# Kernel optimization log

Hardware: AMD Instinct MI355X
Metric: run time of the kernel (lower is better)

Reference implementation:

```python
import jax, jax.numpy as jnp
import numpy as np

RESHAPE = 640
NC = 80
TOPK = 10
EPS = 1e-7      # module eps (BCEloss / log clamps)
IOU_EPS = 1e-9  # iou() eps
DIS = 2.5
BS = 16
NUM_GT = 32


def make_anchors():
    pts, strides = [], []
    for s in (8, 16, 32):
        n = RESHAPE // s
        ys, xs = jnp.meshgrid(jnp.arange(n, dtype=jnp.float32),
                              jnp.arange(n, dtype=jnp.float32), indexing='ij')
        pts.append(jnp.stack([xs.ravel(), ys.ravel()], -1))
        strides.append(jnp.full((n * n, 1), float(s), dtype=jnp.float32))
    return jnp.concatenate(pts, 0), jnp.concatenate(strides, 0)


def setup_inputs() -> dict:
    key = jax.random.key(0)
    ks = jax.random.split(key, 8)
    anchor_points, stride_tensor = make_anchors()
    hw = anchor_points.shape[0]

    def rand_boxes(k, lead):
        k1, k2 = jax.random.split(k)
        c = jax.random.uniform(k1, lead + (2,), minval=80.0, maxval=560.0)
        wh = jax.random.uniform(k2, lead + (2,), minval=20.0, maxval=160.0)
        return jnp.concatenate([c - wh / 2, c + wh / 2], -1)

    pred_boxes = rand_boxes(ks[0], (BS, hw))
    gt_boxes = rand_boxes(ks[1], (BS, NUM_GT))
    counts = jax.random.randint(ks[2], (BS,), 8, NUM_GT + 1)
    mask_gt = jnp.arange(NUM_GT)[None, :] < counts[:, None]
    pred_scores = jax.random.uniform(ks[3], (BS, hw, NC)) * 0.98 + 0.01
    pred_conf = jax.random.uniform(ks[4], (BS, hw, 1)) * 0.98 + 0.01
    gt_labels = jax.random.randint(ks[5], (BS, NUM_GT, 1), 0, NC)
    return dict(pred_boxes=pred_boxes, gt_boxes=gt_boxes, mask_gt=mask_gt,
                pred_scores=pred_scores, pred_conf=pred_conf, gt_labels=gt_labels,
                anchor_points=anchor_points, stride_tensor=stride_tensor)


def box_iou(p, g, ciou=False, eps=IOU_EPS):
    # p, g broadcastable [..., 4] in xyxy; matches the torch iou() exactly
    b1x1, b1y1, b1x2, b1y2 = p[..., 0], p[..., 1], p[..., 2], p[..., 3]
    b2x1, b2y1, b2x2, b2y2 = g[..., 0], g[..., 1], g[..., 2], g[..., 3]
    w1, h1 = b1x2 - b1x1, b1y2 - b1y1 + eps
    w2, h2 = b2x2 - b2x1, b2y2 - b2y1 + eps
    inter = (jnp.maximum(jnp.minimum(b1x2, b2x2) - jnp.maximum(b1x1, b2x1), 0.0)
             * jnp.maximum(jnp.minimum(b1y2, b2y2) - jnp.maximum(b1y1, b2y1), 0.0))
    union = w1 * h1 + w2 * h2 - inter + eps
    iou = inter / union
    if ciou:
        cw = jnp.maximum(b1x2, b2x2) - jnp.minimum(b1x1, b2x1)
        ch = jnp.maximum(b1y2, b2y2) - jnp.minimum(b1y1, b2y1)
        c2 = cw ** 2 + ch ** 2 + eps
        d2 = ((b2x1 + b2x2 - b1x1 - b1x2) ** 2 + (b2y1 + b2y2 - b1y1 - b1y2) ** 2) / 4
        v = (4.0 / np.pi ** 2) * (jnp.arctan(w2 / h2) - jnp.arctan(w1 / h1)) ** 2
        alpha = jax.lax.stop_gradient(v / (v - iou + (1.0 + eps)))
        return iou - (d2 / c2 + v * alpha)
    return iou


def _forward(pred_boxes, gt_boxes, mask_gt, pred_scores, pred_conf, gt_labels,
             anchor_points, stride_tensor):
    bs, hw, nc = pred_scores.shape
    G = mask_gt.shape[1]
    dt = pred_boxes.dtype

    apd = (anchor_points + 0.5) * stride_tensor          # (hw, 2)
    gb = gt_boxes[:, :, None, :]                          # (bs, G, 1, 4)
    # strict in-box test
    lt = apd[None, None] - gb[..., :2]
    rb = gb[..., 2:] - apd[None, None]
    in_boxes = (lt > 0).all(-1) & (rb > 0).all(-1)        # (bs, G, hw)
    # center prior (radius 2.5 * stride)
    ctr = (gb[..., :2] + gb[..., 2:]) / 2
    dis = DIS * stride_tensor                             # (hw, 1) -> broadcast (hw, 2)
    lt2 = apd[None, None] - (ctr - dis)
    rb2 = (ctr + dis) - apd[None, None]
    in_centers = (lt2 > 0).all(-1) & (rb2 > 0).all(-1)
    fg = in_boxes | in_centers
    in_both = in_boxes & in_centers

    iou_val = box_iou(pred_boxes[:, None], gt_boxes[:, :, None])   # (bs, G, hw)
    iou_cost = -jnp.log(iou_val + EPS)

    # torch F.binary_cross_entropy with one-hot target zeroed outside fg:
    # sum_c BCE = S + fg * (nll0[label] - nll1[label]), logs clamped at -100
    nll1 = -jnp.maximum(jnp.log(1.0 - pred_scores), -100.0)        # (bs, hw, nc)
    S = nll1.sum(-1)                                               # (bs, hw)
    bidx = jnp.arange(bs)[:, None, None]
    aidx = jnp.arange(hw)[None, None, :]
    lab = gt_labels[..., 0][:, :, None]
    pl = pred_scores[bidx, aidx, lab]                              # (bs, G, hw)
    nll0_l = -jnp.maximum(jnp.log(pl), -100.0)
    nll1_l = -jnp.maximum(jnp.log(1.0 - pl), -100.0)
    cls_cost = S[:, None] + fg.astype(dt) * (nll0_l - nll1_l)

    cost = cls_cost + 3.0 * iou_cost + 100000.0 * (~in_both).astype(dt)
    cost = jnp.where(mask_gt[:, :, None], cost, jnp.asarray(1e6, dt))

    # dynamic-k: sum of top-min(TOPK, num_fg) ious, floor, clamp(min=1)
    top_iou = jax.lax.top_k(jnp.where(fg, iou_val, -jnp.inf), TOPK)[0]
    pt_num = jnp.maximum(jnp.where(jnp.isfinite(top_iou), top_iou, 0.0).sum(-1),
                         1.0).astype(jnp.int32)
    pt_num = jnp.where(mask_gt, pt_num, 0)                         # invalid gt -> 0

    # pick pt_num smallest-cost anchors per gt via ranks (emulates topk(largest=False))
    ranks = jnp.argsort(jnp.argsort(cost, axis=-1), axis=-1)
    pt_mask = ranks < pt_num[..., None]                            # (bs, G, hw) bool

    # resolve anchors claimed by >1 gt: keep only min-cost gt
    count = pt_mask.sum(1)                                         # (bs, hw)
    best = jnp.argmin(cost, axis=1)                                # (bs, hw)
    onehot = best[:, None, :] == jnp.arange(G)[None, :, None]
    pt_mask = jnp.where(count[:, None] > 1, onehot, pt_mask)

    m = pt_mask.astype(dt)
    num_pts = m.sum((1, 2))                                        # (bs,)

    ciou_v = box_iou(pred_boxes[:, None], gt_boxes[:, :, None], ciou=True)
    l0 = (((1.0 - ciou_v) * m).sum((1, 2)) / num_pts).sum()

    # module BCEloss (with EPS) vs one-hot target, summed over classes
    Se = (-jnp.log(1.0 - pred_scores + EPS)).sum(-1)               # (bs, hw)
    bce = Se[:, None] + (-jnp.log(pl + EPS)) - (-jnp.log(1.0 - pl + EPS))
    l1 = ((bce * m).sum((1, 2)) / num_pts).sum()

    gt_conf = (pt_mask.sum(1) > 0).astype(dt)                      # (bs, hw)
    pc = pred_conf[..., 0]
    bce_c = -gt_conf * jnp.log(pc + EPS) - (1.0 - gt_conf) * jnp.log(1.0 - pc + EPS)
    l2 = (bce_c.sum(-1) / num_pts).sum()
    return l0, l1, l2


def reference(pred_boxes, gt_boxes, mask_gt, pred_scores, pred_conf, gt_labels,
              anchor_points, stride_tensor):
    return _forward(pred_boxes, gt_boxes, mask_gt, pred_scores, pred_conf,
                    gt_labels, anchor_points, stride_tensor)
```

## Files before the change

kernel.cpp:

```cpp
#include <hip/hip_runtime.h>
#include <math.h>

#define TPB 256
#define KTOP 10
#define GMAX 32
#define NITER 33

__device__ __forceinline__ bool read_maskgt(const void* p, int i) {
    const unsigned char* b = (const unsigned char*)p;
    if (b[1] != 0) return b[i] != 0;
    return ((const int*)p)[i] != 0;
}

__global__ void k0_init(float* out, int* numpts, float* bce_sum, int bs) {
    int t = threadIdx.x;
    if (t < 3) out[t] = 0.0f;
    if (t < bs) { numpts[t] = 0; bce_sum[t] = 0.0f; }
}

__global__ void k2a_cost(const float* __restrict__ pred_boxes,
                         const float* __restrict__ gt_boxes,
                         const void*  mask_gt,
                         const float* __restrict__ ps,
                         const int*   __restrict__ labels,
                         const float* __restrict__ anchors,
                         const float* __restrict__ strides,
                         float* __restrict__ Se,
                         float* __restrict__ cost,
                         unsigned char* __restrict__ mask,
                         unsigned char* __restrict__ best,
                         int G, int HW, int NC) {
    __shared__ float4 s_gb[GMAX];
    __shared__ float  s_ctrx[GMAX], s_ctry[GMAX];
    __shared__ int    s_lab[GMAX];
    __shared__ int    s_val[GMAX];

    int b = blockIdx.y;
    int tid = threadIdx.x;
    if (tid < G) {
        int pr = b * G + tid;
        float4 gb = ((const float4*)gt_boxes)[pr];
        s_gb[tid] = gb;
        s_ctrx[tid] = (gb.x + gb.z) * 0.5f;
        s_ctry[tid] = (gb.y + gb.w) * 0.5f;
        s_lab[tid] = labels[pr];
        s_val[tid] = read_maskgt(mask_gt, pr) ? 1 : 0;
    }
    __syncthreads();

    int a = blockIdx.x * TPB + tid;
    if (a >= HW) return;

    const float* __restrict__ row = ps + ((long)b * HW + a) * NC;
    float Sa = 0.f, se = 0.f;
    int c = 0;
    for (; c + 4 <= NC; c += 4) {
        float4 v = *(const float4*)(row + c);
        Sa += -fmaxf(logf(1.0f - v.x), -100.0f) - fmaxf(logf(1.0f - v.y), -100.0f)
            - fmaxf(logf(1.0f - v.z), -100.0f) - fmaxf(logf(1.0f - v.w), -100.0f);
        se += -logf(1.0f - v.x + 1e-7f) - logf(1.0f - v.y + 1e-7f)
            - logf(1.0f - v.z + 1e-7f) - logf(1.0f - v.w + 1e-7f);
    }
    for (; c < NC; ++c) {
        float p = row[c];
        Sa += -fmaxf(logf(1.0f - p), -100.0f);
        se += -logf(1.0f - p + 1e-7f);
    }
    Se[(long)b * HW + a] = se;

    const float4 pb = ((const float4*)(pred_boxes + (long)b * HW * 4))[a];
    float ax = anchors[2 * a], ay = anchors[2 * a + 1];
    float st = strides[a];
    float apx = (ax + 0.5f) * st, apy = (ay + 0.5f) * st;
    float dis = 2.5f * st;
    float w1 = pb.z - pb.x, h1 = pb.w - pb.y + 1e-9f;
    float w1h1 = w1 * h1;

    float bestc = 3.4e38f;
    int bestg = 0;

#pragma unroll
    for (int g = 0; g < GMAX; ++g) {
        if (g >= G) break;
        long oidx = ((long)(b * G + g)) * HW + a;
        float cst;
        if (!s_val[g]) {
            cst = 1e6f;
        } else {
            float pl = row[s_lab[g]];
            float4 gb = s_gb[g];
            float gx1 = gb.x, gy1 = gb.y, gx2 = gb.z, gy2 = gb.w;
            bool in_boxes = (apx - gx1 > 0.f) & (apy - gy1 > 0.f) &
                            (gx2 - apx > 0.f) & (gy2 - apy > 0.f);
            float ctrx = s_ctrx[g], ctry = s_ctry[g];
            bool in_centers = (apx - (ctrx - dis) > 0.f) & (apy - (ctry - dis) > 0.f) &
                              ((ctrx + dis) - apx > 0.f) & ((ctry + dis) - apy > 0.f);
            bool fg = in_boxes | in_centers;
            bool in_both = in_boxes & in_centers;

            float w2 = gx2 - gx1, h2 = gy2 - gy1 + 1e-9f;
            float iw = fminf(pb.z, gx2) - fmaxf(pb.x, gx1);
            float ih = fminf(pb.w, gy2) - fmaxf(pb.y, gy1);
            float inter = fmaxf(iw, 0.f) * fmaxf(ih, 0.f);
            float uni = w1h1 + w2 * h2 - inter + 1e-9f;
            float iou = inter / uni;
            float iou_cost = -logf(iou + 1e-7f);

            float nll0 = -fmaxf(logf(pl), -100.f);
            float nll1 = -fmaxf(logf(1.f - pl), -100.f);
            float cls = Sa + (fg ? (nll0 - nll1) : 0.f);
            cst = cls + 3.f * iou_cost + (in_both ? 0.f : 100000.f);
        }
        cost[oidx] = cst;
        mask[oidx] = 0;
        if (cst < bestc) { bestc = cst; bestg = g; }
    }
    best[(long)b * HW + a] = (unsigned char)bestg;
}

__device__ __forceinline__ void radix_sel(const unsigned* keys, int kth,
                                          unsigned* s_hist, int* s_bin, int* s_cum,
                                          int tid, unsigned& outKey, int& outCnt) {
    unsigned pref = 0;
    int kk = kth, cnt = 0;
#pragma unroll
    for (int lvl = 0; lvl < 4; ++lvl) {
        const int sh = 24 - 8 * lvl;
        s_hist[tid] = 0u;
        __syncthreads();
        int curBin = -1; unsigned curCnt = 0u;
#pragma unroll
        for (int j = 0; j < NITER; ++j) {
            unsigned key = keys[j];
            bool par = (lvl == 0) || ((key >> (sh + 8)) == pref);
            if (par) {
                int d = (int)((key >> sh) & 255u);
                if (d == curBin) curCnt++;
                else {
                    if (curBin >= 0) atomicAdd(&s_hist[curBin], curCnt);
                    curBin = d; curCnt = 1u;
                }
            }
        }
        if (curBin >= 0) atomicAdd(&s_hist[curBin], curCnt);
        __syncthreads();
        if (tid < 64) {
            unsigned h0 = s_hist[4 * tid + 0], h1 = s_hist[4 * tid + 1];
            unsigned h2 = s_hist[4 * tid + 2], h3 = s_hist[4 * tid + 3];
            int tot = (int)(h0 + h1 + h2 + h3);
            int incl = tot;
            for (int off = 1; off < 64; off <<= 1) {
                int o = __shfl_up(incl, off);
                if (tid >= off) incl += o;
            }
            int ex = incl - tot;
            bool hit = (ex < kk) && (incl >= kk);
            unsigned long long bal = __ballot(hit);
            int src = __ffsll((unsigned long long)bal) - 1;
            if (tid == src) {
                int c = ex; int bsel = 4 * tid;
                if (c + (int)h0 < kk) { c += (int)h0; bsel++;
                    if (c + (int)h1 < kk) { c += (int)h1; bsel++;
                        if (c + (int)h2 < kk) { c += (int)h2; bsel++; } } }
                *s_bin = bsel; *s_cum = c;
            }
        }
        __syncthreads();
        int bin = *s_bin, c = *s_cum;
        kk -= c; cnt += c;
        pref = (pref << 8) | (unsigned)bin;
        __syncthreads();
    }
    outKey = pref; outCnt = cnt;
}

__global__ void k2_sel(const float* __restrict__ pred_boxes,
                       const float* __restrict__ gt_boxes,
                       const void*  mask_gt,
                       const float* __restrict__ anchors,
                       const float* __restrict__ strides,
                       const float* __restrict__ cost,
                       unsigned char* __restrict__ mask,
                       int G, int HW) {
    __shared__ unsigned s_hist[256];
    __shared__ int s_bin, s_cum;
    __shared__ float s_red[256];
    __shared__ int s_ptn;
    __shared__ unsigned s_tie[256];
    __shared__ int s_tiecnt;

    int pair = blockIdx.x;
    if (!read_maskgt(mask_gt, pair)) return;
    int b = pair / G;
    int tid = threadIdx.x;

    const float4 gb = ((const float4*)gt_boxes)[pair];
    const float gx1 = gb.x, gy1 = gb.y, gx2 = gb.z, gy2 = gb.w;
    const float ctrx = (gx1 + gx2) * 0.5f, ctry = (gy1 + gy2) * 0.5f;
    const float w2 = gx2 - gx1, h2 = gy2 - gy1 + 1e-9f;

    const float* pbb  = pred_boxes + (long)b * HW * 4;
    const float* crow = cost + (long)pair * HW;

    unsigned ck[NITER], ik[NITER];
#pragma unroll
    for (int j = 0; j < NITER; ++j) {
        int a = j * TPB + tid;
        unsigned ckey = 0xFFFFFFFFu, ikey = 0xFFFFFFFFu;
        if (a < HW) {
            float4 pb = ((const float4*)pbb)[a];
            float ax = anchors[2 * a], ay = anchors[2 * a + 1];
            float st = strides[a];
            float apx = (ax + 0.5f) * st, apy = (ay + 0.5f) * st;
            bool in_boxes = (apx - gx1 > 0.f) & (apy - gy1 > 0.f) &
                            (gx2 - apx > 0.f) & (gy2 - apy > 0.f);
            float dis = 2.5f * st;
            bool in_centers = (apx - (ctrx - dis) > 0.f) & (apy - (ctry - dis) > 0.f) &
                              ((ctrx + dis) - apx > 0.f) & ((ctry + dis) - apy > 0.f);
            bool fg = in_boxes | in_centers;

            float w1 = pb.z - pb.x, h1 = pb.w - pb.y + 1e-9f;
            float iw = fminf(pb.z, gx2) - fmaxf(pb.x, gx1);
            float ih = fminf(pb.w, gy2) - fmaxf(pb.y, gy1);
            float inter = fmaxf(iw, 0.f) * fmaxf(ih, 0.f);
            float uni = w1 * h1 + w2 * h2 - inter + 1e-9f;
            float iou = inter / uni;

            float c = crow[a];
            unsigned cb = __float_as_uint(c);
            ckey = cb ^ (((int)cb < 0) ? 0xFFFFFFFFu : 0x80000000u);
            ikey = fg ? ~__float_as_uint(iou) : 0xFFFFFFFFu;
        }
        ck[j] = ckey; ik[j] = ikey;
    }

    unsigned K10; int cnt10;
    radix_sel(ik, KTOP, s_hist, &s_bin, &s_cum, tid, K10, cnt10);

    float ls = 0.f;
#pragma unroll
    for (int j = 0; j < NITER; ++j)
        if (ik[j] < K10) ls += __uint_as_float(~ik[j]);
    s_red[tid] = ls;
    __syncthreads();
    for (int s = 128; s; s >>= 1) {
        if (tid < s) s_red[tid] += s_red[tid + s];
        __syncthreads();
    }
    if (tid == 0) {
        float tot = s_red[0] + (float)(KTOP - cnt10) * __uint_as_float(~K10);
        s_ptn = (int)fmaxf(tot, 1.0f);
    }
    __syncthreads();
    int ptn = s_ptn;

    unsigned Kc; int cntc;
    radix_sel(ck, ptn, s_hist, &s_bin, &s_cum, tid, Kc, cntc);
    int tneed = ptn - cntc;

    if (tid == 0) s_tiecnt = 0;
    __syncthreads();
    unsigned char* mrow = mask + (long)pair * HW;
#pragma unroll
    for (int j = 0; j < NITER; ++j) {
        int a = j * TPB + tid;
        if (a < HW) {
            if (ck[j] < Kc) mrow[a] = 1;
            else if (ck[j] == Kc) {
                int p = atomicAdd(&s_tiecnt, 1);
                if (p < 256) s_tie[p] = (unsigned)a;
            }
        }
    }
    __syncthreads();
    int m = min(s_tiecnt, 256);
    if (tneed >= m) {
        for (int e = tid; e < m; e += TPB) mrow[s_tie[e]] = 1;
    } else if (tneed > 0) {
        for (int e = tid; e < m; e += TPB) {
            unsigned my = s_tie[e];
            int r = 0;
            for (int q = 0; q < m; ++q) r += (s_tie[q] < my) ? 1 : 0;
            if (r < tneed) mrow[my] = 1;
        }
    }
}

__global__ void k3_assign(const unsigned char* __restrict__ best,
                          const float* __restrict__ pred_conf,
                          unsigned char* __restrict__ mask,
                          int* __restrict__ numpts,
                          float* __restrict__ bce_sum,
                          int G, int HW) {
    __shared__ int   red[TPB];
    __shared__ float redf[TPB];
    int b = blockIdx.y;
    int a = blockIdx.x * TPB + threadIdx.x;
    int cntf = 0;
    float vbce = 0.f;
    if (a < HW) {
        int cnt = 0;
        for (int g = 0; g < G; ++g)
            cnt += mask[((long)(b * G + g)) * HW + a];
        if (cnt > 1) {
            unsigned int bits = 1u << best[(long)b * HW + a];
            for (int g = 0; g < G; ++g)
                mask[((long)(b * G + g)) * HW + a] = (unsigned char)((bits >> g) & 1u);
        }
        cntf = (cnt > 1) ? 1 : cnt;
        float pc = pred_conf[(long)b * HW + a];
        vbce = (cntf > 0) ? -logf(pc + 1e-7f) : -logf(1.f - pc + 1e-7f);
    }
    red[threadIdx.x] = cntf;
    redf[threadIdx.x] = vbce;
    __syncthreads();
    for (int s = TPB / 2; s; s >>= 1) {
        if (threadIdx.x < s) {
            red[threadIdx.x]  += red[threadIdx.x + s];
            redf[threadIdx.x] += redf[threadIdx.x + s];
        }
        __syncthreads();
    }
    if (threadIdx.x == 0) {
        if (red[0] > 0) atomicAdd(&numpts[b], red[0]);
        atomicAdd(&bce_sum[b], redf[0]);
    }
}

__global__ void k4_pair(const float* __restrict__ pred_boxes,
                        const float* __restrict__ gt_boxes,
                        const float* __restrict__ ps,
                        const int*   __restrict__ labels,
                        const float* __restrict__ Se,
                        const unsigned char* __restrict__ mask,
                        const int* __restrict__ numpts,
                        const float* __restrict__ bce_sum,
                        float* __restrict__ out,
                        int G, int HW, int NC) {
    __shared__ float r0[TPB];
    __shared__ float r1[TPB];
    int tid = threadIdx.x;
    int pair = blockIdx.x;
    int b = pair / G;
    const unsigned char* mrow = mask + (long)pair * HW;
    const float4 gb = ((const float4*)gt_boxes)[pair];
    float gx1 = gb.x, gy1 = gb.y, gx2 = gb.z, gy2 = gb.w;
    float w2 = gx2 - gx1, h2 = gy2 - gy1 + 1e-9f;
    int lab = labels[pair];
    const float* pbb   = pred_boxes + (long)b * HW * 4;
    const float* psb   = ps + (long)b * HW * NC;
    const float* Serow = Se + (long)b * HW;
    float at2 = atanf(w2 / h2);
    float s0 = 0.f, s1 = 0.f;
    for (int a = tid; a < HW; a += TPB) {
        if (!mrow[a]) continue;
        float4 pb = ((const float4*)pbb)[a];
        float w1 = pb.z - pb.x, h1 = pb.w - pb.y + 1e-9f;
        float iw = fminf(pb.z, gx2) - fmaxf(pb.x, gx1);
        float ih = fminf(pb.w, gy2) - fmaxf(pb.y, gy1);
        float inter = fmaxf(iw, 0.f) * fmaxf(ih, 0.f);
        float uni = w1 * h1 + w2 * h2 - inter + 1e-9f;
        float iou = inter / uni;
        float cw = fmaxf(pb.z, gx2) - fminf(pb.x, gx1);
        float ch = fmaxf(pb.w, gy2) - fminf(pb.y, gy1);
        float c2 = cw * cw + ch * ch + 1e-9f;
        float dx = gx1 + gx2 - pb.x - pb.z;
        float dy = gy1 + gy2 - pb.y - pb.w;
        float d2 = (dx * dx + dy * dy) * 0.25f;
        float dat = at2 - atanf(w1 / h1);
        float v = 0.4052847345693511f * dat * dat;
        float alpha = v / (v - iou + 1.0f);
        float ciou = iou - (d2 / c2 + v * alpha);
        s0 += 1.0f - ciou;
        float pl = psb[(long)a * NC + lab];
        s1 += Serow[a] - logf(pl + 1e-7f) + logf(1.f - pl + 1e-7f);
    }
    r0[tid] = s0; r1[tid] = s1;
    __syncthreads();
    for (int s = TPB / 2; s; s >>= 1) {
        if (tid < s) { r0[tid] += r0[tid + s]; r1[tid] += r1[tid + s]; }
        __syncthreads();
    }
    if (tid == 0) {
        float np = (float)numpts[b];
        if (r0[0] != 0.f || r1[0] != 0.f) {
            atomicAdd(out + 0, r0[0] / np);
            atomicAdd(out + 1, r1[0] / np);
        }
        if ((pair % G) == 0)
            atomicAdd(out + 2, bce_sum[b] / np);
    }
}

extern "C" void kernel_launch(void* const* d_in, const int* in_sizes, int n_in,
                              void* d_out, int out_size, void* d_ws, size_t ws_size,
                              hipStream_t stream) {
    const float* pred_boxes = (const float*)d_in[0];
    const float* gt_boxes   = (const float*)d_in[1];
    const void*  mask_gt    = d_in[2];
    const float* ps         = (const float*)d_in[3];
    const float* pred_conf  = (const float*)d_in[4];
    const int*   gt_labels  = (const int*)d_in[5];
    const float* anchors    = (const float*)d_in[6];
    const float* strides    = (const float*)d_in[7];
    float* out = (float*)d_out;

    const int HW = in_sizes[7];
    const int BS = in_sizes[4] / HW;
    const int G  = in_sizes[5] / BS;
    const int NC = in_sizes[3] / (BS * HW);

    char* w = (char*)d_ws;
    float* Se = (float*)w;                    w += (size_t)BS * HW * 4;
    float* cost = (float*)w;                  w += (size_t)BS * G * HW * 4;
    int* numpts = (int*)w;                    w += 256;
    float* bce_sum = (float*)w;               w += 256;
    unsigned char* mask = (unsigned char*)w;  w += (size_t)BS * G * HW;
    unsigned char* best = (unsigned char*)w;

    k0_init<<<1, 64, 0, stream>>>(out, numpts, bce_sum, BS);

    dim3 g2a((HW + TPB - 1) / TPB, BS);
    k2a_cost<<<g2a, TPB, 0, stream>>>(pred_boxes, gt_boxes, mask_gt, ps, gt_labels,
                                      anchors, strides, Se, cost, mask, best, G, HW, NC);

    k2_sel<<<BS * G, TPB, 0, stream>>>(pred_boxes, gt_boxes, mask_gt, anchors,
                                       strides, cost, mask, G, HW);

    dim3 g3((HW + TPB - 1) / TPB, BS);
    k3_assign<<<g3, TPB, 0, stream>>>(best, pred_conf, mask, numpts, bce_sum, G, HW);

    k4_pair<<<BS * G, TPB, 0, stream>>>(pred_boxes, gt_boxes, ps, gt_labels, Se,
                                        mask, numpts, bce_sum, out, G, HW, NC);
}
```

Baseline: 200.8 us.

## Split each anchor's cost computation across four lanes with shuffle reductions

Measured after the change: 196.5 us. -2.2%, faster.

```diff
diff --git a/kernel.cpp b/kernel.cpp
--- a/kernel.cpp
+++ b/kernel.cpp
@@ -48,25 +48,37 @@
     }
     __syncthreads();
 
-    int a = blockIdx.x * TPB + tid;
+    int q = tid & 3;
+    int a = blockIdx.x * (TPB / 4) + (tid >> 2);
     if (a >= HW) return;
 
     const float* __restrict__ row = ps + ((long)b * HW + a) * NC;
+    int nper = NC / 4;
+    int c0 = q * nper;
     float Sa = 0.f, se = 0.f;
-    int c = 0;
-    for (; c + 4 <= NC; c += 4) {
+    int c = c0;
+    for (; c + 4 <= c0 + nper; c += 4) {
         float4 v = *(const float4*)(row + c);
         Sa += -fmaxf(logf(1.0f - v.x), -100.0f) - fmaxf(logf(1.0f - v.y), -100.0f)
             - fmaxf(logf(1.0f - v.z), -100.0f) - fmaxf(logf(1.0f - v.w), -100.0f);
         se += -logf(1.0f - v.x + 1e-7f) - logf(1.0f - v.y + 1e-7f)
             - logf(1.0f - v.z + 1e-7f) - logf(1.0f - v.w + 1e-7f);
     }
-    for (; c < NC; ++c) {
+    for (; c < c0 + nper; ++c) {
         float p = row[c];
         Sa += -fmaxf(logf(1.0f - p), -100.0f);
         se += -logf(1.0f - p + 1e-7f);
     }
-    Se[(long)b * HW + a] = se;
+    if (q == 3) {
+        for (int cc = 4 * nper; cc < NC; ++cc) {
+            float p = row[cc];
+            Sa += -fmaxf(logf(1.0f - p), -100.0f);
+            se += -logf(1.0f - p + 1e-7f);
+        }
+    }
+    Sa += __shfl_xor(Sa, 1); se += __shfl_xor(se, 1);
+    Sa += __shfl_xor(Sa, 2); se += __shfl_xor(se, 2);
+    if (q == 0) Se[(long)b * HW + a] = se;
 
     const float4 pb = ((const float4*)(pred_boxes + (long)b * HW * 4))[a];
     float ax = anchors[2 * a], ay = anchors[2 * a + 1];
@@ -77,10 +89,11 @@
     float w1h1 = w1 * h1;
 
     float bestc = 3.4e38f;
-    int bestg = 0;
-
-#pragma unroll
-    for (int g = 0; g < GMAX; ++g) {
+    int bestg = 0x7fffffff;
+
+#pragma unroll
+    for (int gi = 0; gi < GMAX / 4; ++gi) {
+        int g = q + 4 * gi;
         if (g >= G) break;
         long oidx = ((long)(b * G + g)) * HW + a;
         float cst;
@@ -113,9 +126,15 @@
         }
         cost[oidx] = cst;
         mask[oidx] = 0;
-        if (cst < bestc) { bestc = cst; bestg = g; }
-    }
-    best[(long)b * HW + a] = (unsigned char)bestg;
+        if (cst < bestc || (cst == bestc && g < bestg)) { bestc = cst; bestg = g; }
+    }
+    {
+        float oc = __shfl_xor(bestc, 1); int og = __shfl_xor(bestg, 1);
+        if (oc < bestc || (oc == bestc && og < bestg)) { bestc = oc; bestg = og; }
+        oc = __shfl_xor(bestc, 2); og = __shfl_xor(bestg, 2);
+        if (oc < bestc || (oc == bestc && og < bestg)) { bestc = oc; bestg = og; }
+    }
+    if (q == 0) best[(long)b * HW + a] = (unsigned char)bestg;
 }
 
 __device__ __forceinline__ void radix_sel(const unsigned* keys, int kth,
@@ -420,7 +439,7 @@
 
     k0_init<<<1, 64, 0, stream>>>(out, numpts, bce_sum, BS);
 
-    dim3 g2a((HW + TPB - 1) / TPB, BS);
+    dim3 g2a((HW + TPB / 4 - 1) / (TPB / 4), BS);
     k2a_cost<<<g2a, TPB, 0, stream>>>(pred_boxes, gt_boxes, mask_gt, ps, gt_labels,
                                       anchors, strides, Se, cost, mask, best, G, HW, NC);
 
```
